# Kernel tuning notes

Hardware: AMD Instinct MI355X
Metric: run time of the kernel (lower is better)

The kernel has to match this reference:

```python
import jax, jax.numpy as jnp
import numpy as np

HID, AA, ESM = 128, 21, 320
D1 = HID + AA + ESM          # 469
N_GRAPHS = 64
BN_EPS = 1e-5


def _lin_params(key, din, dout):
    k1, k2 = jax.random.split(key)
    s = 1.0 / np.sqrt(din)
    W = jax.random.uniform(k1, (din, dout), jnp.float32, -s, s)
    b = jax.random.uniform(k2, (dout,), jnp.float32, -s, s)
    return W, b


def setup_inputs() -> dict:
    key = jax.random.key(0)
    ks = jax.random.split(key, 16)
    N, E = 30000, 480000
    inp = {
        'prot_x': jax.random.normal(ks[0], (N, 6485), jnp.float32),
        'prot_edge_index': jax.random.randint(ks[1], (2, E), 0, N, jnp.int64),
        'prot_batch': jnp.sort(jax.random.randint(ks[2], (N,), 0, N_GRAPHS, jnp.int64)),
    }
    inp['fl1_W'], inp['fl1_b'] = _lin_params(ks[3], 6165 - 21, HID)
    inp['fl2_W'], inp['fl2_b'] = _lin_params(ks[4], AA, AA)
    inp['fl3_W'], inp['fl3_b'] = _lin_params(ks[5], ESM, ESM)
    inp['pdb1_W'], inp['pdb1_b'] = _lin_params(ks[6], D1, D1)
    inp['pdb2_W'], inp['pdb2_b'] = _lin_params(ks[7], D1, 2 * D1)
    inp['af1_W'], inp['af1_b'] = _lin_params(ks[8], D1, D1)
    inp['af2_W'], inp['af2_b'] = _lin_params(ks[9], D1, 2 * D1)
    inp['pdb3_W'], inp['pdb3_b'] = _lin_params(ks[10], 4 * D1, 4 * D1)
    inp['fc1_W'], inp['fc1_b'] = _lin_params(ks[11], 4 * D1, 1024)
    inp['bn_g'] = jnp.ones((1024,), jnp.float32)
    inp['bn_b'] = jnp.zeros((1024,), jnp.float32)
    inp['fc2_W'], inp['fc2_b'] = _lin_params(ks[12], 1024, 486)
    return inp


def _gcn_graph(edge_index, n):
    # add self-loops, symmetric normalization D^-1/2 (A+I) D^-1/2
    loops = jnp.arange(n, dtype=edge_index.dtype)
    src = jnp.concatenate([edge_index[0], loops])
    dst = jnp.concatenate([edge_index[1], loops])
    deg = jax.ops.segment_sum(jnp.ones_like(dst, jnp.float32), dst, n)
    dinv = jax.lax.rsqrt(jnp.maximum(deg, 1.0))  # deg >= 1 via self-loop
    norm = dinv[src] * dinv[dst]
    return src, dst, norm


def _gcn_conv(x, W, b, src, dst, norm, n):
    h = x @ W                                   # [N, Dout]
    msg = h[src] * norm[:, None]                # gather + scale
    return jax.ops.segment_sum(msg, dst, n) + b  # scatter-add


def reference(prot_x, prot_edge_index, prot_batch,
              fl1_W, fl1_b, fl2_W, fl2_b, fl3_W, fl3_b,
              pdb1_W, pdb1_b, pdb2_W, pdb2_b,
              af1_W, af1_b, af2_W, af2_b,
              pdb3_W, pdb3_b, fc1_W, fc1_b, bn_g, bn_b, fc2_W, fc2_b):
    n = prot_x.shape[0]
    relu = jax.nn.relu
    f1 = relu(prot_x[:, 21:6165] @ fl1_W + fl1_b)   # [N,128]
    f2 = relu(prot_x[:, :21] @ fl2_W + fl2_b)       # [N,21]
    f3 = relu(prot_x[:, 6165:] @ fl3_W + fl3_b)     # [N,320]
    feat = jnp.concatenate([f2, f1, f3], axis=1)    # [N,469]

    src, dst, norm = _gcn_graph(prot_edge_index, n)
    x = relu(_gcn_conv(feat, pdb1_W, pdb1_b, src, dst, norm, n))
    x = relu(_gcn_conv(x, pdb2_W, pdb2_b, src, dst, norm, n))
    y = relu(_gcn_conv(feat, af1_W, af1_b, src, dst, norm, n))
    y = relu(_gcn_conv(y, af2_W, af2_b, src, dst, norm, n))
    z = jnp.concatenate([x, y], axis=1)             # [N, 4*469]
    z = relu(_gcn_conv(z, pdb3_W, pdb3_b, src, dst, norm, n))

    # gap: global mean pool per graph
    cnt = jax.ops.segment_sum(jnp.ones((n,), jnp.float32), prot_batch, N_GRAPHS)
    z = jax.ops.segment_sum(z, prot_batch, N_GRAPHS) / jnp.maximum(cnt, 1.0)[:, None]

    z = z @ fc1_W + fc1_b                            # [G,1024]
    mu = jnp.mean(z, axis=0)
    var = jnp.mean((z - mu) ** 2, axis=0)            # biased, torch BN training math
    z = (z - mu) * jax.lax.rsqrt(var + BN_EPS) * bn_g + bn_b
    z = relu(z)                                      # dropout = identity (eval)
    z = z @ fc2_W + fc2_b
    return jax.nn.sigmoid(z)
```

## Files before the change

kernel.cpp:

```cpp
#include <hip/hip_runtime.h>
#include <hip/hip_bf16.h>
#include <stdint.h>

#define NG 64

typedef __attribute__((ext_vector_type(8))) short bf16x8;
typedef __attribute__((ext_vector_type(4))) float f32x4;

#define AS1 __attribute__((address_space(1)))
#define AS3 __attribute__((address_space(3)))

static __device__ __forceinline__ unsigned short f2b(float f) {
    unsigned u = __float_as_uint(f);
    return (unsigned short)((u + 0x7fffu + ((u >> 16) & 1u)) >> 16);
}
static __device__ __forceinline__ float b2f(unsigned short h) {
    return __uint_as_float(((unsigned)h) << 16);
}
static __device__ __forceinline__ void gl16(const void* g, void* l) {
    __builtin_amdgcn_global_load_lds(
        (const AS1 void*)(uintptr_t)g,
        (AS3 void*)(unsigned)(uintptr_t)l, 16, 0, 0);
}

__global__ void initcnt_k(int* cnt, int n) {
    int i = blockIdx.x * blockDim.x + threadIdx.x;
    if (i < n) cnt[i] = 0;
}
__global__ void count_k(const int* __restrict__ dst, int* cnt, int E) {
    int e = blockIdx.x * blockDim.x + threadIdx.x;
    if (e < E) atomicAdd(&cnt[dst[e]], 1);
}
__global__ void scan1_k(const int* __restrict__ cnt, int* __restrict__ scan,
                        int* __restrict__ bsum, int n) {
    __shared__ int wsum[16];
    int tid = threadIdx.x, lane = tid & 63, wid = tid >> 6;
    int i = blockIdx.x * 1024 + tid;
    int x = (i < n) ? cnt[i] : 0;
#pragma unroll
    for (int off = 1; off < 64; off <<= 1) {
        int t = __shfl_up(x, off);
        if (lane >= off) x += t;
    }
    if (lane == 63) wsum[wid] = x;
    __syncthreads();
    if (tid < 16) {
        int s = wsum[tid];
#pragma unroll
        for (int off = 1; off < 16; off <<= 1) {
            int t = __shfl_up(s, off);
            if (tid >= off) s += t;
        }
        wsum[tid] = s;
    }
    __syncthreads();
    int add = wid ? wsum[wid - 1] : 0;
    if (i < n) scan[i] = x + add;
    if (tid == 1023) bsum[blockIdx.x] = x + add;
}
__global__ void scan2_k(int* bsum, int nb) {
    int tid = threadIdx.x;
    int x = (tid < nb) ? bsum[tid] : 0;
#pragma unroll
    for (int off = 1; off < 64; off <<= 1) {
        int t = __shfl_up(x, off);
        if (tid >= off) x += t;
    }
    if (tid < nb) bsum[tid] = x;
}
__global__ void scan3f_k(const int* __restrict__ scan, const int* __restrict__ bsum,
                         const int* __restrict__ cnt,
                         int* __restrict__ rowptr, int* __restrict__ fill,
                         float* __restrict__ dinv, int n) {
    int i = blockIdx.x * blockDim.x + threadIdx.x;
    if (i >= n) return;
    int b = i >> 10;
    int rp1 = scan[i] + (b ? bsum[b - 1] : 0);
    rowptr[i + 1] = rp1;
    int rp0 = rp1 - cnt[i];
    if (i == 0) rowptr[0] = 0;
    fill[i] = rp0;
    dinv[i] = rsqrtf((float)(cnt[i] + 1));
}
__global__ void fill_k(const int* __restrict__ src, const int* __restrict__ dst,
                       int* fill, int* csr, int E) {
    int e = blockIdx.x * blockDim.x + threadIdx.x;
    if (e < E) {
        int d = dst[e];
        int pos = atomicAdd(&fill[d], 1);
        csr[pos] = src[e];
    }
}

__global__ void wtconv_k(const float* __restrict__ W, int K, int Nout,
                         unsigned short* __restrict__ Wt, int Kpad, int Nrows, int remap) {
    __shared__ float t[32][33];
    int k0 = blockIdx.x * 32, n0 = blockIdx.y * 32;
    int cx = threadIdx.x & 31, ry = threadIdx.x >> 5;
#pragma unroll
    for (int p = 0; p < 4; ++p) {
        int k = k0 + ry + p * 8, nn = n0 + cx;
        int ko = k;
        bool kvalid;
        if (remap) {
            ko = (k < 448) ? k + 21 : k - 448;
            kvalid = (k < 469);
        } else {
            kvalid = (k < K);
        }
        t[ry + p * 8][cx] = (kvalid && nn < Nout) ? W[(size_t)ko * Nout + nn] : 0.0f;
    }
    __syncthreads();
#pragma unroll
    for (int p = 0; p < 4; ++p) {
        int nn = n0 + ry + p * 8, k = k0 + cx;
        if (nn < Nrows) Wt[(size_t)nn * Kpad + k] = f2b(t[cx][ry + p * 8]);
    }
}

__global__ void biascat_k(const float* __restrict__ b0, const float* __restrict__ b1,
                          float* __restrict__ out) {
    int i = threadIdx.x + blockIdx.x * blockDim.x;
    if (i >= 960) return;
    int seg = i >= 480, c = i - seg * 480;
    const float* b = seg ? b1 : b0;
    out[i] = (c < 469) ? b[c] : 0.0f;
}

__global__ void fl2_k(const float* __restrict__ x, int ldx,
                      const float* __restrict__ W, const float* __restrict__ b,
                      unsigned short* __restrict__ out, int ldo, int n) {
    __shared__ float Ws[441];
    __shared__ float Bs[21];
    int tid = threadIdx.x;
    for (int i = tid; i < 441; i += 256) Ws[i] = W[i];
    if (tid < 21) Bs[tid] = b[tid];
    __syncthreads();
    int row = blockIdx.x * 256 + tid;
    if (row >= n) return;
    float xv[21];
#pragma unroll
    for (int j = 0; j < 21; ++j) xv[j] = x[(size_t)row * ldx + j];
    for (int c = 0; c < 32; ++c) {
        float v = 0.0f;
        if (c < 21) {
            float a = Bs[c];
#pragma unroll
            for (int j = 0; j < 21; ++j) a = fmaf(xv[j], Ws[j * 21 + c], a);
            v = fmaxf(a, 0.0f);
        }
        out[(size_t)row * ldo + 448 + c] = f2b(v);
    }
}

template<int NI, bool A32>
__global__ __launch_bounds__(256) void mgemm_t(
    const void* __restrict__ Aptr, int lda, int Mreal,
    const unsigned short* __restrict__ Bt, int ldb,
    const float* __restrict__ bias,
    unsigned short* __restrict__ C, int ldc, int coff,
    int K, int Nout, int Nzero, int GX) {
    constexpr int BNT = NI * 32;
    __shared__ unsigned short As[128 * 32];
    __shared__ unsigned short Bs[BNT * 32];
    const int tid = threadIdx.x;
    const int w = tid >> 6, lane = tid & 63;

    const int nwg = gridDim.x;
    const int q = nwg >> 3, r = nwg & 7;
    const int xcd = blockIdx.x & 7, oidx = blockIdx.x >> 3;
    const int swz = (xcd < r ? xcd * (q + 1) : r * (q + 1) + (xcd - r) * q) + oidx;
    const int m0 = (swz / GX) * 128, n0 = (swz % GX) * BNT;

    const int wr = w >> 1, wc = w & 1;

    f32x4 acc[4][NI];
#pragma unroll
    for (int i = 0; i < 4; ++i)
#pragma unroll
        for (int j = 0; j < NI; ++j) acc[i][j] = (f32x4){0.f, 0.f, 0.f, 0.f};

    const int ko = (lane >> 4) * 8;
    const int rA = wr * 64 + (lane & 15);
    const int rB = wc * (NI * 16) + (lane & 15);

    for (int k0 = 0; k0 < K; k0 += 32) {
        if constexpr (A32) {
            const float* Af = (const float*)Aptr;
#pragma unroll
            for (int j = 0; j < 2; ++j) {
                int c = w * 2 + j;
                int id2 = c * 64 + lane;
                int row = id2 >> 2, cc = id2 & 3;
                int gm = m0 + row; if (gm > Mreal - 1) gm = Mreal - 1;
                const float* ap = Af + (size_t)gm * lda + k0 + cc * 8;
                float4 v0 = *(const float4*)ap;
                float4 v1 = *(const float4*)(ap + 4);
                unsigned short t[8] = {f2b(v0.x), f2b(v0.y), f2b(v0.z), f2b(v0.w),
                                       f2b(v1.x), f2b(v1.y), f2b(v1.z), f2b(v1.w)};
                *(bf16x8*)&As[row * 32 + cc * 8] = *(const bf16x8*)t;
            }
        } else {
            const unsigned short* Ab = (const unsigned short*)Aptr;
#pragma unroll
            for (int j = 0; j < 2; ++j) {
                int c = w * 2 + j;
                int id2 = c * 64 + lane;
                int row = id2 >> 2, cc = id2 & 3;
                gl16(Ab + (size_t)(m0 + row) * lda + k0 + cc * 8, &As[c * 512]);
            }
        }
#pragma unroll
        for (int j = 0; j < NI / 2; ++j) {
            int c = w * (NI / 2) + j;
            int id2 = c * 64 + lane;
            int row = id2 >> 2, cc = id2 & 3;
            gl16(Bt + (size_t)(n0 + row) * ldb + k0 + cc * 8, &Bs[c * 512]);
        }
        __syncthreads();
        bf16x8 a[4], b[NI];
#pragma unroll
        for (int i = 0; i < 4; ++i) a[i] = *(const bf16x8*)&As[(rA + i * 16) * 32 + ko];
#pragma unroll
        for (int j = 0; j < NI; ++j) b[j] = *(const bf16x8*)&Bs[(rB + j * 16) * 32 + ko];
#pragma unroll
        for (int i = 0; i < 4; ++i)
#pragma unroll
            for (int j = 0; j < NI; ++j)
                acc[i][j] = __builtin_amdgcn_mfma_f32_16x16x32_bf16(a[i], b[j], acc[i][j], 0, 0, 0);
        __syncthreads();
    }

    const int cn = lane & 15, r4 = (lane >> 4) * 4;
    for (int ni = 0; ni < NI; ++ni) {
        int col = n0 + wc * (NI * 16) + ni * 16 + cn;
        if (col >= Nzero) continue;
        bool real = col < Nout;
        float bb = real ? bias[col] : 0.0f;
#pragma unroll
        for (int mi = 0; mi < 4; ++mi) {
#pragma unroll
            for (int rr = 0; rr < 4; ++rr) {
                int row = m0 + wr * 64 + mi * 16 + r4 + rr;
                float x = real ? fmaxf(acc[mi][ni][rr] + bb, 0.0f) : 0.0f;
                C[(size_t)row * ldc + coff + col] = f2b(x);
            }
        }
    }
}

__global__ __launch_bounds__(256) void fl1part_k(
    const float* __restrict__ A, int lda, int Mreal,
    const unsigned short* __restrict__ Bt, int ldb,
    float* __restrict__ part, int MT, int Mpad) {
    __shared__ unsigned short As[128 * 32];
    __shared__ unsigned short Bs[128 * 32];
    const int tid = threadIdx.x;
    const int w = tid >> 6, lane = tid & 63;
    const int mt = blockIdx.x % MT, ks = blockIdx.x / MT;
    const int m0 = mt * 128;
    const int kbeg = ks * 2048, kend = kbeg + 2048;
    const int wr = w >> 1, wc = w & 1;

    f32x4 acc[4][4];
#pragma unroll
    for (int i = 0; i < 4; ++i)
#pragma unroll
        for (int j = 0; j < 4; ++j) acc[i][j] = (f32x4){0.f, 0.f, 0.f, 0.f};

    const int ko = (lane >> 4) * 8;
    const int rA = wr * 64 + (lane & 15);
    const int rB = wc * 64 + (lane & 15);

    for (int k0 = kbeg; k0 < kend; k0 += 32) {
#pragma unroll
        for (int j = 0; j < 2; ++j) {
            int c = w * 2 + j;
            int id2 = c * 64 + lane;
            int row = id2 >> 2, cc = id2 & 3;
            int gm = m0 + row; if (gm > Mreal - 1) gm = Mreal - 1;
            const float* ap = A + (size_t)gm * lda + k0 + cc * 8;
            float4 v0 = *(const float4*)ap;
            float4 v1 = *(const float4*)(ap + 4);
            unsigned short t[8] = {f2b(v0.x), f2b(v0.y), f2b(v0.z), f2b(v0.w),
                                   f2b(v1.x), f2b(v1.y), f2b(v1.z), f2b(v1.w)};
            *(bf16x8*)&As[row * 32 + cc * 8] = *(const bf16x8*)t;
            gl16(Bt + (size_t)row * ldb + k0 + cc * 8, &Bs[c * 512]);
        }
        __syncthreads();
        bf16x8 a[4], b[4];
#pragma unroll
        for (int i = 0; i < 4; ++i) a[i] = *(const bf16x8*)&As[(rA + i * 16) * 32 + ko];
#pragma unroll
        for (int j = 0; j < 4; ++j) b[j] = *(const bf16x8*)&Bs[(rB + j * 16) * 32 + ko];
#pragma unroll
        for (int i = 0; i < 4; ++i)
#pragma unroll
            for (int j = 0; j < 4; ++j)
                acc[i][j] = __builtin_amdgcn_mfma_f32_16x16x32_bf16(a[i], b[j], acc[i][j], 0, 0, 0);
        __syncthreads();
    }

    float* pb = part + (size_t)ks * Mpad * 128;
    const int cn = lane & 15, r4 = (lane >> 4) * 4;
#pragma unroll
    for (int ni = 0; ni < 4; ++ni) {
        int col = wc * 64 + ni * 16 + cn;
#pragma unroll
        for (int mi = 0; mi < 4; ++mi) {
#pragma unroll
            for (int rr = 0; rr < 4; ++rr) {
                int row = m0 + wr * 64 + mi * 16 + r4 + rr;
                pb[(size_t)row * 128 + col] = acc[mi][ni][rr];
            }
        }
    }
}

__global__ void fl1red_k(const float* __restrict__ part, const float* __restrict__ bias,
                         unsigned short* __restrict__ feat, int Mpad) {
    int i = blockIdx.x * blockDim.x + threadIdx.x;
    if (i >= Mpad * 32) return;
    int row = i >> 5, c = (i & 31) * 4;
    size_t base = (size_t)row * 128 + c;
    size_t stride = (size_t)Mpad * 128;
    float4 p0 = *(const float4*)(part + base);
    float4 p1 = *(const float4*)(part + stride + base);
    float4 p2 = *(const float4*)(part + 2 * stride + base);
    float4 bb = *(const float4*)(bias + c);
    ushort4 o;
    o.x = f2b(fmaxf(p0.x + p1.x + p2.x + bb.x, 0.0f));
    o.y = f2b(fmaxf(p0.y + p1.y + p2.y + bb.y, 0.0f));
    o.z = f2b(fmaxf(p0.z + p1.z + p2.z + bb.z, 0.0f));
    o.w = f2b(fmaxf(p0.w + p1.w + p2.w + bb.w, 0.0f));
    *(ushort4*)(feat + (size_t)row * 480 + c) = o;
}

__global__ __launch_bounds__(256) void agg_wave_k(
    const unsigned short* __restrict__ in, unsigned short* __restrict__ out,
    const float* __restrict__ dinv, const int* __restrict__ rowptr,
    const int* __restrict__ csr, int D8, int ld, int n) {
    int lane = threadIdx.x & 63;
    int node = blockIdx.x * 4 + (threadIdx.x >> 6);
    if (node >= n) return;
    bool act = lane < D8;
    float di = dinv[node];
    float acc[8];
#pragma unroll
    for (int t = 0; t < 8; ++t) acc[t] = 0.0f;
    if (act) {
        bf16x8 v = *(const bf16x8*)(in + (size_t)node * ld + lane * 8);
#pragma unroll
        for (int t = 0; t < 8; ++t) acc[t] = di * b2f((unsigned short)v[t]);
    }
    int s = rowptr[node], e = rowptr[node + 1];
    for (int c = s; c < e; c += 64) {
        int m = e - c; if (m > 64) m = 64;
        int idx = (c + lane < e) ? csr[c + lane] : 0;
        float wl = dinv[idx];
        for (int j = 0; j < m; ++j) {
            int src = __shfl(idx, j);
            float wgt = __shfl(wl, j);
            if (act) {
                bf16x8 v = *(const bf16x8*)(in + (size_t)src * ld + lane * 8);
#pragma unroll
                for (int t = 0; t < 8; ++t) acc[t] = fmaf(wgt, b2f((unsigned short)v[t]), acc[t]);
            }
        }
    }
    if (act) {
        unsigned short o[8];
#pragma unroll
        for (int t = 0; t < 8; ++t) o[t] = f2b(di * acc[t]);
        *(bf16x8*)(out + (size_t)node * ld + lane * 8) = *(const bf16x8*)o;
    }
}

__global__ void agg_block_k(
    const unsigned short* __restrict__ in, unsigned short* __restrict__ out,
    const float* __restrict__ dinv, const int* __restrict__ rowptr,
    const int* __restrict__ csr, int D8, int ld, int n) {
    int i = blockIdx.x;
    int tid = threadIdx.x;
    __shared__ int s_src[64];
    __shared__ float s_w[64];
    bool act = tid < D8;
    float di = dinv[i];
    float acc[8];
#pragma unroll
    for (int t = 0; t < 8; ++t) acc[t] = 0.0f;
    if (act) {
        bf16x8 v = *(const bf16x8*)(in + (size_t)i * ld + tid * 8);
#pragma unroll
        for (int t = 0; t < 8; ++t) acc[t] = di * b2f((unsigned short)v[t]);
    }
    int s = rowptr[i], e = rowptr[i + 1];
    for (int c = s; c < e; c += 64) {
        int k = c + tid;
        if (tid < 64 && k < e) { int sn = csr[k]; s_src[tid] = sn; s_w[tid] = dinv[sn]; }
        __syncthreads();
        int m = e - c; if (m > 64) m = 64;
        for (int j = 0; j < m; ++j) {
            int sn = s_src[j];
            float wgt = s_w[j];
            if (act) {
                bf16x8 v = *(const bf16x8*)(in + (size_t)sn * ld + tid * 8);
#pragma unroll
                for (int t = 0; t < 8; ++t) acc[t] = fmaf(wgt, b2f((unsigned short)v[t]), acc[t]);
            }
        }
        __syncthreads();
    }
    if (act) {
        unsigned short o[8];
#pragma unroll
        for (int t = 0; t < 8; ++t) o[t] = f2b(di * acc[t]);
        *(bf16x8*)(out + (size_t)i * ld + tid * 8) = *(const bf16x8*)o;
    }
}

__global__ void pool_k(const unsigned short* __restrict__ in, int ld,
                       const int* __restrict__ batch,
                       float* __restrict__ out, int n, int D) {
    int g = blockIdx.y;
    int d8 = blockIdx.x * blockDim.x + threadIdx.x;
    if (d8 * 8 >= ld) return;
    int lo = 0, hi = n;
    while (lo < hi) { int mid = (lo + hi) >> 1; if (batch[mid] < g) lo = mid + 1; else hi = mid; }
    int start = lo;
    lo = start; hi = n;
    while (lo < hi) { int mid = (lo + hi) >> 1; if (batch[mid] < g + 1) lo = mid + 1; else hi = mid; }
    int end = lo;
    float s[8];
#pragma unroll
    for (int j = 0; j < 8; ++j) s[j] = 0.0f;
#pragma unroll 4
    for (int r = start; r < end; r++) {
        bf16x8 v = *(const bf16x8*)(in + (size_t)r * ld + d8 * 8);
#pragma unroll
        for (int j = 0; j < 8; ++j) s[j] += b2f((unsigned short)v[j]);
    }
    float inv = 1.0f / fmaxf((float)(end - start), 1.0f);
#pragma unroll
    for (int j = 0; j < 8; ++j) {
        int d = d8 * 8 + j;
        if (d < D) out[(size_t)g * D + d] = s[j] * inv;
    }
}

__global__ __launch_bounds__(256) void sgemm_part_k(
    const float* __restrict__ A, int lda,
    const float* __restrict__ W, int ldw,
    float* __restrict__ part, int K, int Nout, int ksplit) {
    const int n0 = blockIdx.x * 64;
    const int ks = blockIdx.y;
    const int kbeg = (int)(((long long)K * ks) / ksplit);
    const int kend = (int)(((long long)K * (ks + 1)) / ksplit);
    const int tx = threadIdx.x & 63, ty = threadIdx.x >> 6;
    __shared__ float As[64][65];
    float acc[16];
#pragma unroll
    for (int r = 0; r < 16; ++r) acc[r] = 0.0f;

    for (int kb = kbeg; kb < kend; kb += 64) {
        int kc = kend - kb; if (kc > 64) kc = 64;
        for (int i = threadIdx.x; i < 64 * 64; i += 256) {
            int r = i >> 6, c = i & 63;
            As[r][c] = (c < kc) ? A[(size_t)r * lda + kb + c] : 0.0f;
        }
        __syncthreads();
        if (n0 + tx < Nout) {
            for (int k = 0; k < kc; ++k) {
                float w = W[(size_t)(kb + k) * ldw + n0 + tx];
#pragma unroll
                for (int r = 0; r < 16; ++r)
                    acc[r] = fmaf(As[ty * 16 + r][k], w, acc[r]);
            }
        }
        __syncthreads();
    }
    if (n0 + tx < Nout) {
#pragma unroll
        for (int r = 0; r < 16; ++r)
            part[((size_t)ks * 64 + ty * 16 + r) * Nout + n0 + tx] = acc[r];
    }
}

__global__ void sgemm_reduce_k(const float* __restrict__ part, const float* __restrict__ bias,
                               float* __restrict__ C, int ldc, int Nout, int ksplit, int act) {
    int i = blockIdx.x * blockDim.x + threadIdx.x;
    if (i >= NG * Nout) return;
    int m = i / Nout, n = i - m * Nout;
    float v = bias[n];
    for (int s = 0; s < ksplit; ++s) v += part[((size_t)s * 64 + m) * Nout + n];
    if (act == 2) v = 1.0f / (1.0f + expf(-v));
    C[(size_t)m * ldc + n] = v;
}

__global__ void bn_k(const float* __restrict__ z, const float* __restrict__ g,
                     const float* __restrict__ b, float* __restrict__ out) {
    int c = blockIdx.x * blockDim.x + threadIdx.x;
    if (c >= 1024) return;
    float s = 0.0f, s2 = 0.0f;
    for (int r = 0; r < NG; r++) { float v = z[r * 1024 + c]; s += v; s2 += v * v; }
    float mu = s / (float)NG;
    float var = s2 / (float)NG - mu * mu;
    float sc = g[c] * rsqrtf(var + 1e-5f);
    float sh = b[c] - mu * sc;
    for (int r = 0; r < NG; r++)
        out[r * 1024 + c] = fmaxf(fmaf(z[r * 1024 + c], sc, sh), 0.0f);
}

extern "C" void kernel_launch(void* const* d_in, const int* in_sizes, int n_in,
                              void* d_out, int out_size, void* d_ws, size_t ws_size,
                              hipStream_t stream) {
    (void)n_in; (void)out_size; (void)ws_size;
    const float* prot_x = (const float*)d_in[0];
    const int*   eidx   = (const int*)d_in[1];
    const int*   batch  = (const int*)d_in[2];
    const float* fl1_W = (const float*)d_in[3],  *fl1_b = (const float*)d_in[4];
    const float* fl2_W = (const float*)d_in[5],  *fl2_b = (const float*)d_in[6];
    const float* fl3_W = (const float*)d_in[7],  *fl3_b = (const float*)d_in[8];
    const float* pdb1_W = (const float*)d_in[9],  *pdb1_b = (const float*)d_in[10];
    const float* pdb2_W = (const float*)d_in[11], *pdb2_b = (const float*)d_in[12];
    const float* af1_W  = (const float*)d_in[13], *af1_b  = (const float*)d_in[14];
    const float* af2_W  = (const float*)d_in[15], *af2_b  = (const float*)d_in[16];
    const float* pdb3_W = (const float*)d_in[17], *pdb3_b = (const float*)d_in[18];
    const float* fc1_W  = (const float*)d_in[19], *fc1_b  = (const float*)d_in[20];
    const float* bn_g   = (const float*)d_in[21], *bn_b   = (const float*)d_in[22];
    const float* fc2_W  = (const float*)d_in[23], *fc2_b  = (const float*)d_in[24];

    const int N = in_sizes[2];
    const int E = in_sizes[1] / 2;
    const int* e_src = eidx;
    const int* e_dst = eidx + E;
    const int Mpad = ((N + 127) / 128) * 128;
    const int MT = Mpad / 128;
    const int NB = (N + 1023) / 1024;

    char* wp = (char*)d_ws;
    auto alloc = [&](size_t bytes) -> char* {
        char* r = wp; wp += (bytes + 255) & ~(size_t)255; return r;
    };
    unsigned short* feat = (unsigned short*)alloc((size_t)Mpad * 480 * 2);
    unsigned short* tmp1 = (unsigned short*)alloc((size_t)Mpad * 480 * 2);
    unsigned short* hxy  = (unsigned short*)alloc((size_t)Mpad * 960 * 2);
    unsigned short* tmp2 = (unsigned short*)alloc((size_t)Mpad * 960 * 2);
    unsigned short* zb   = (unsigned short*)alloc((size_t)Mpad * 1920 * 2);
    unsigned short* zagg = (unsigned short*)alloc((size_t)Mpad * 1920 * 2);
    unsigned short* zout = (unsigned short*)alloc((size_t)Mpad * 1888 * 2);
    unsigned short* wt_fl1  = (unsigned short*)alloc((size_t)128 * 6144 * 2);
    unsigned short* wt_fl3  = (unsigned short*)alloc((size_t)384 * 320 * 2);
    unsigned short* wt_c1   = (unsigned short*)alloc((size_t)1024 * 480 * 2);
    unsigned short* wt_pdb2 = (unsigned short*)alloc((size_t)1024 * 480 * 2);
    unsigned short* wt_af2  = (unsigned short*)alloc((size_t)1152 * 480 * 2);
    unsigned short* wt_pdb3 = (unsigned short*)alloc((size_t)1920 * 1920 * 2);
    float* f_bias1 = (float*)alloc(960 * 4);
    float* f_dinv = (float*)alloc((size_t)N * 4);
    float* f_pool = (float*)alloc((size_t)NG * 1876 * 4);
    float* f_fc1  = (float*)alloc((size_t)NG * 1024 * 4);
    float* f_bn   = (float*)alloc((size_t)NG * 1024 * 4);
    float* f_part = (float*)alloc((size_t)16 * 64 * 1024 * 4);
    float* f_flp  = (float*)alloc((size_t)3 * Mpad * 128 * 4);
    int* i_cnt    = (int*)alloc((size_t)N * 4);
    int* i_scan   = (int*)alloc((size_t)N * 4);
    int* i_bsum   = (int*)alloc(64 * 4);
    int* i_rowptr = (int*)alloc((size_t)(N + 1) * 4);
    int* i_fill   = (int*)alloc((size_t)N * 4);
    int* i_csr    = (int*)alloc((size_t)E * 4);

    auto mg = [&](const unsigned short* A, int lda, const unsigned short* Wt, int ldb,
                  const float* bias, unsigned short* C, int ldc, int coff,
                  int K, int Nout, int Nzero) {
        int gx = (Nzero + 191) / 192;
        mgemm_t<6, false><<<gx * MT, 256, 0, stream>>>(
            A, lda, Mpad, Wt, ldb, bias, C, ldc, coff, K, Nout, Nzero, gx);
    };
    auto mgf = [&](const float* A, int lda, const unsigned short* Wt, int ldb,
                   const float* bias, unsigned short* C, int ldc, int coff,
                   int K, int Nout, int Nzero) {
        int gx = (Nzero + 127) / 128;
        mgemm_t<4, true><<<gx * MT, 256, 0, stream>>>(
            A, lda, N, Wt, ldb, bias, C, ldc, coff, K, Nout, Nzero, gx);
    };
    auto wt = [&](const float* W, int K, int Nout, unsigned short* Wt, int Kpad, int Nrows, int remap) {
        wtconv_k<<<dim3(Kpad / 32, Nrows / 32), 256, 0, stream>>>(W, K, Nout, Wt, Kpad, Nrows, remap);
    };

    initcnt_k<<<(N + 255) / 256, 256, 0, stream>>>(i_cnt, N);
    count_k<<<(E + 255) / 256, 256, 0, stream>>>(e_dst, i_cnt, E);
    scan1_k<<<NB, 1024, 0, stream>>>(i_cnt, i_scan, i_bsum, N);
    scan2_k<<<1, 64, 0, stream>>>(i_bsum, NB);
    scan3f_k<<<(N + 255) / 256, 256, 0, stream>>>(i_scan, i_bsum, i_cnt, i_rowptr, i_fill, f_dinv, N);
    fill_k<<<(E + 255) / 256, 256, 0, stream>>>(e_src, e_dst, i_fill, i_csr, E);

    wt(fl1_W, 6144, 128, wt_fl1, 6144, 128, 0);
    wt(fl3_W, 320, 320, wt_fl3, 320, 384, 0);
    wt(pdb1_W, 469, 469, wt_c1, 480, 480, 1);
    wt(af1_W, 469, 469, wt_c1 + (size_t)480 * 480, 480, 544, 1);
    wt(pdb2_W, 469, 938, wt_pdb2, 480, 1024, 0);
    wt(af2_W, 469, 938, wt_af2, 480, 1152, 0);
    wt(pdb3_W, 1876, 1876, wt_pdb3, 1920, 1920, 0);
    biascat_k<<<4, 256, 0, stream>>>(pdb1_b, af1_b, f_bias1);

    fl2_k<<<(N + 255) / 256, 256, 0, stream>>>(prot_x, 6485, fl2_W, fl2_b, feat, 480, N);
    fl1part_k<<<MT * 3, 256, 0, stream>>>(prot_x + 21, 6485, N, wt_fl1, 6144, f_flp, MT, Mpad);
    fl1red_k<<<(Mpad * 32 + 255) / 256, 256, 0, stream>>>(f_flp, fl1_b, feat, Mpad);
    mgf(prot_x + 6165, 6485, wt_fl3, 320, fl3_b, feat, 480, 128, 320, 320, 320);

    agg_wave_k<<<(N + 3) / 4, 256, 0, stream>>>(feat, tmp1, f_dinv, i_rowptr, i_csr, 60, 480, N);
    mg(tmp1, 480, wt_c1, 480, f_bias1, hxy, 960, 0, 480, 960, 960);
    agg_block_k<<<N, 128, 0, stream>>>(hxy, tmp2, f_dinv, i_rowptr, i_csr, 120, 960, N);
    mg(tmp2,       960, wt_pdb2, 480, pdb2_b, zb, 1920, 0,   480, 938, 938);
    mg(tmp2 + 480, 960, wt_af2,  480, af2_b,  zb, 1920, 938, 480, 938, 982);
    agg_block_k<<<N, 256, 0, stream>>>(zb, zagg, f_dinv, i_rowptr, i_csr, 240, 1920, N);
    mg(zagg, 1920, wt_pdb3, 1920, pdb3_b, zout, 1888, 0, 1920, 1876, 1888);

    pool_k<<<dim3(4, NG), 64, 0, stream>>>(zout, 1888, batch, f_pool, N, 1876);
    sgemm_part_k<<<dim3(16, 16), 256, 0, stream>>>(f_pool, 1876, fc1_W, 1024, f_part, 1876, 1024, 16);
    sgemm_reduce_k<<<(NG * 1024 + 255) / 256, 256, 0, stream>>>(f_part, fc1_b, f_fc1, 1024, 1024, 16, 0);
    bn_k<<<4, 256, 0, stream>>>(f_fc1, bn_g, bn_b, f_bn);
    sgemm_part_k<<<dim3(8, 16), 256, 0, stream>>>(f_bn, 1024, fc2_W, 486, f_part, 1024, 486, 16);
    sgemm_reduce_k<<<(NG * 486 + 255) / 256, 256, 0, stream>>>(f_part, fc2_b, (float*)d_out, 486, 486, 16, 2);
}
```

Before: 1.574 ms.

## Merge weight-prep launches, raise fl1 split-K to four, widen fl3 GEMM tile

The seven weight transpose/convert launches and the bias-concat launch become one `wprep_k` kernel that works out its weight matrix from a block-index range, which cuts per-launch overhead. The fl1 split-K goes from 3 slices of 2048 to 4 slices of 1536, adding blocks to spread the large fp32 input stream across more CUs. The reduction kernel now sums four partials, and the partial buffer grows to match. The fl3 GEMM switches from the 4-wide to the 6-wide template tile, giving fewer, larger blocks.

```diff
diff --git a/kernel.cpp b/kernel.cpp
--- a/kernel.cpp
+++ b/kernel.cpp
@@ -92,39 +92,53 @@
     }
 }
 
-__global__ void wtconv_k(const float* __restrict__ W, int K, int Nout,
-                         unsigned short* __restrict__ Wt, int Kpad, int Nrows, int remap) {
+__global__ void wprep_k(const float* __restrict__ fl1W, const float* __restrict__ fl3W,
+                        const float* __restrict__ p1W, const float* __restrict__ a1W,
+                        const float* __restrict__ p2W, const float* __restrict__ a2W,
+                        const float* __restrict__ p3W,
+                        unsigned short* __restrict__ t_fl1, unsigned short* __restrict__ t_fl3,
+                        unsigned short* __restrict__ t_c1, unsigned short* __restrict__ t_p2,
+                        unsigned short* __restrict__ t_a2, unsigned short* __restrict__ t_p3,
+                        const float* __restrict__ p1b, const float* __restrict__ a1b,
+                        float* __restrict__ bias1) {
+    int bid = blockIdx.x;
+    if (bid >= 5988) {
+        int i = (bid - 5988) * 256 + threadIdx.x;
+        if (i < 960) {
+            int seg = i >= 480, c = i - seg * 480;
+            const float* b = seg ? a1b : p1b;
+            bias1[i] = (c < 469) ? b[c] : 0.0f;
+        }
+        return;
+    }
+    const float* W; unsigned short* Wt; int K, Nout, Kpad, remap, local;
+    if (bid < 768)       { W = fl1W; Wt = t_fl1; K = 6144; Nout = 128;  Kpad = 6144; remap = 0; local = bid; }
+    else if (bid < 888)  { W = fl3W; Wt = t_fl3; K = 320;  Nout = 320;  Kpad = 320;  remap = 0; local = bid - 768; }
+    else if (bid < 1113) { W = p1W;  Wt = t_c1;  K = 469;  Nout = 469;  Kpad = 480;  remap = 1; local = bid - 888; }
+    else if (bid < 1368) { W = a1W;  Wt = t_c1 + (size_t)480 * 480; K = 469; Nout = 469; Kpad = 480; remap = 1; local = bid - 1113; }
+    else if (bid < 1848) { W = p2W;  Wt = t_p2;  K = 469;  Nout = 938;  Kpad = 480;  remap = 0; local = bid - 1368; }
+    else if (bid < 2388) { W = a2W;  Wt = t_a2;  K = 469;  Nout = 938;  Kpad = 480;  remap = 0; local = bid - 1848; }
+    else                 { W = p3W;  Wt = t_p3;  K = 1876; Nout = 1876; Kpad = 1920; remap = 0; local = bid - 2388; }
+    int ktiles = Kpad >> 5;
+    int k0 = (local % ktiles) * 32, n0 = (local / ktiles) * 32;
+
     __shared__ float t[32][33];
-    int k0 = blockIdx.x * 32, n0 = blockIdx.y * 32;
     int cx = threadIdx.x & 31, ry = threadIdx.x >> 5;
 #pragma unroll
     for (int p = 0; p < 4; ++p) {
         int k = k0 + ry + p * 8, nn = n0 + cx;
         int ko = k;
         bool kvalid;
-        if (remap) {
-            ko = (k < 448) ? k + 21 : k - 448;
-            kvalid = (k < 469);
-        } else {
-            kvalid = (k < K);
-        }
+        if (remap) { ko = (k < 448) ? k + 21 : k - 448; kvalid = (k < 469); }
+        else       { kvalid = (k < K); }
         t[ry + p * 8][cx] = (kvalid && nn < Nout) ? W[(size_t)ko * Nout + nn] : 0.0f;
     }
     __syncthreads();
 #pragma unroll
     for (int p = 0; p < 4; ++p) {
         int nn = n0 + ry + p * 8, k = k0 + cx;
-        if (nn < Nrows) Wt[(size_t)nn * Kpad + k] = f2b(t[cx][ry + p * 8]);
-    }
-}
-
-__global__ void biascat_k(const float* __restrict__ b0, const float* __restrict__ b1,
-                          float* __restrict__ out) {
-    int i = threadIdx.x + blockIdx.x * blockDim.x;
-    if (i >= 960) return;
-    int seg = i >= 480, c = i - seg * 480;
-    const float* b = seg ? b1 : b0;
-    out[i] = (c < 469) ? b[c] : 0.0f;
+        Wt[(size_t)nn * Kpad + k] = f2b(t[cx][ry + p * 8]);
+    }
 }
 
 __global__ void fl2_k(const float* __restrict__ x, int ldx,
@@ -259,7 +273,7 @@
     const int w = tid >> 6, lane = tid & 63;
     const int mt = blockIdx.x % MT, ks = blockIdx.x / MT;
     const int m0 = mt * 128;
-    const int kbeg = ks * 2048, kend = kbeg + 2048;
+    const int kbeg = ks * 1536, kend = kbeg + 1536;
     const int wr = w >> 1, wc = w & 1;
 
     f32x4 acc[4][4];
@@ -327,12 +341,13 @@
     float4 p0 = *(const float4*)(part + base);
     float4 p1 = *(const float4*)(part + stride + base);
     float4 p2 = *(const float4*)(part + 2 * stride + base);
+    float4 p3 = *(const float4*)(part + 3 * stride + base);
     float4 bb = *(const float4*)(bias + c);
     ushort4 o;
-    o.x = f2b(fmaxf(p0.x + p1.x + p2.x + bb.x, 0.0f));
-    o.y = f2b(fmaxf(p0.y + p1.y + p2.y + bb.y, 0.0f));
-    o.z = f2b(fmaxf(p0.z + p1.z + p2.z + bb.z, 0.0f));
-    o.w = f2b(fmaxf(p0.w + p1.w + p2.w + bb.w, 0.0f));
+    o.x = f2b(fmaxf(p0.x + p1.x + p2.x + p3.x + bb.x, 0.0f));
+    o.y = f2b(fmaxf(p0.y + p1.y + p2.y + p3.y + bb.y, 0.0f));
+    o.z = f2b(fmaxf(p0.z + p1.z + p2.z + p3.z + bb.z, 0.0f));
+    o.w = f2b(fmaxf(p0.w + p1.w + p2.w + p3.w + bb.w, 0.0f));
     *(ushort4*)(feat + (size_t)row * 480 + c) = o;
 }
 
@@ -561,7 +576,7 @@
     float* f_fc1  = (float*)alloc((size_t)NG * 1024 * 4);
     float* f_bn   = (float*)alloc((size_t)NG * 1024 * 4);
     float* f_part = (float*)alloc((size_t)16 * 64 * 1024 * 4);
-    float* f_flp  = (float*)alloc((size_t)3 * Mpad * 128 * 4);
+    float* f_flp  = (float*)alloc((size_t)4 * Mpad * 128 * 4);
     int* i_cnt    = (int*)alloc((size_t)N * 4);
     int* i_scan   = (int*)alloc((size_t)N * 4);
     int* i_bsum   = (int*)alloc(64 * 4);
@@ -576,15 +591,12 @@
         mgemm_t<6, false><<<gx * MT, 256, 0, stream>>>(
             A, lda, Mpad, Wt, ldb, bias, C, ldc, coff, K, Nout, Nzero, gx);
     };
-    auto mgf = [&](const float* A, int lda, const unsigned short* Wt, int ldb,
-                   const float* bias, unsigned short* C, int ldc, int coff,
-                   int K, int Nout, int Nzero) {
-        int gx = (Nzero + 127) / 128;
-        mgemm_t<4, true><<<gx * MT, 256, 0, stream>>>(
+    auto mgf6 = [&](const float* A, int lda, const unsigned short* Wt, int ldb,
+                    const float* bias, unsigned short* C, int ldc, int coff,
+                    int K, int Nout, int Nzero) {
+        int gx = (Nzero + 191) / 192;
+        mgemm_t<6, true><<<gx * MT, 256, 0, stream>>>(
             A, lda, N, Wt, ldb, bias, C, ldc, coff, K, Nout, Nzero, gx);
-    };
-    auto wt = [&](const float* W, int K, int Nout, unsigned short* Wt, int Kpad, int Nrows, int remap) {
-        wtconv_k<<<dim3(Kpad / 32, Nrows / 32), 256, 0, stream>>>(W, K, Nout, Wt, Kpad, Nrows, remap);
     };
 
     initcnt_k<<<(N + 255) / 256, 256, 0, stream>>>(i_cnt, N);
@@ -594,19 +606,14 @@
     scan3f_k<<<(N + 255) / 256, 256, 0, stream>>>(i_scan, i_bsum, i_cnt, i_rowptr, i_fill, f_dinv, N);
     fill_k<<<(E + 255) / 256, 256, 0, stream>>>(e_src, e_dst, i_fill, i_csr, E);
 
-    wt(fl1_W, 6144, 128, wt_fl1, 6144, 128, 0);
-    wt(fl3_W, 320, 320, wt_fl3, 320, 384, 0);
-    wt(pdb1_W, 469, 469, wt_c1, 480, 480, 1);
-    wt(af1_W, 469, 469, wt_c1 + (size_t)480 * 480, 480, 544, 1);
-    wt(pdb2_W, 469, 938, wt_pdb2, 480, 1024, 0);
-    wt(af2_W, 469, 938, wt_af2, 480, 1152, 0);
-    wt(pdb3_W, 1876, 1876, wt_pdb3, 1920, 1920, 0);
-    biascat_k<<<4, 256, 0, stream>>>(pdb1_b, af1_b, f_bias1);
+    wprep_k<<<5992, 256, 0, stream>>>(fl1_W, fl3_W, pdb1_W, af1_W, pdb2_W, af2_W, pdb3_W,
+                                      wt_fl1, wt_fl3, wt_c1, wt_pdb2, wt_af2, wt_pdb3,
+                                      pdb1_b, af1_b, f_bias1);
 
     fl2_k<<<(N + 255) / 256, 256, 0, stream>>>(prot_x, 6485, fl2_W, fl2_b, feat, 480, N);
-    fl1part_k<<<MT * 3, 256, 0, stream>>>(prot_x + 21, 6485, N, wt_fl1, 6144, f_flp, MT, Mpad);
+    fl1part_k<<<MT * 4, 256, 0, stream>>>(prot_x + 21, 6485, N, wt_fl1, 6144, f_flp, MT, Mpad);
     fl1red_k<<<(Mpad * 32 + 255) / 256, 256, 0, stream>>>(f_flp, fl1_b, feat, Mpad);
-    mgf(prot_x + 6165, 6485, wt_fl3, 320, fl3_b, feat, 480, 128, 320, 320, 320);
+    mgf6(prot_x + 6165, 6485, wt_fl3, 320, fl3_b, feat, 480, 128, 320, 320, 320);
 
     agg_wave_k<<<(N + 3) / 4, 256, 0, stream>>>(feat, tmp1, f_dinv, i_rowptr, i_csr, 60, 480, N);
     mg(tmp1, 480, wt_c1, 480, f_bias1, hxy, 960, 0, 480, 960, 960);
```

New measurement: 1.639 ms. 4.1% more time.
